# Kernel optimization log

Hardware: AMD Instinct MI355X
Metric: run time of the kernel (lower is better)

Reference implementation:

```python
import jax, jax.numpy as jnp
import numpy as np

D = 768      # d_model == d_patch (16*16*3)
DFF = 3072
NH = 12
DH = D // NH  # 64
P = 16
IMG = 224
HP = IMG // P  # 14
NP = HP * HP   # 196
L = NP + 1     # 197 with CLS
NL = 12        # layers (weights SHARED across layers, per original code)
NC = 1000


def _pos_enc(length, d):
    # Faithful to PositionalEncoding: even dims sin with exponent i, odd dims cos with exponent i-1
    pos = jnp.arange(length, dtype=jnp.float32)[:, None]          # [L,1]
    dim = jnp.arange(d)
    i = jnp.where(dim % 2 == 0, dim, (dim // 2) * 2).astype(jnp.float32)
    ang = pos / jnp.power(10000.0, i / d)                          # [L,D]
    return jnp.where(dim % 2 == 0, jnp.sin(ang), jnp.cos(ang))


def _ln(x, g, b, eps=1e-5):
    m = x.mean(-1, keepdims=True)
    v = x.var(-1, keepdims=True)
    return (x - m) / jnp.sqrt(v + eps) * g + b


def setup_inputs() -> dict:
    key = jax.random.key(0)
    ks = jax.random.split(key, 12)
    s = 0.02
    n = lambda k, shp: jax.random.normal(k, shp, jnp.float32) * s
    return {
        "x": jax.random.normal(ks[0], (32, 3, IMG, IMG), jnp.float32),
        "w_proj": n(ks[1], (D, D)), "b_proj": jnp.zeros((D,), jnp.float32),
        "cls_emb": jnp.zeros((1, 1, D), jnp.float32),
        "ln1_g": jnp.ones((D,), jnp.float32), "ln1_b": jnp.zeros((D,), jnp.float32),
        "w_qkv": n(ks[2], (3 * D, D)), "b_qkv": jnp.zeros((3 * D,), jnp.float32),
        "w_o": n(ks[3], (D, D)), "b_o": jnp.zeros((D,), jnp.float32),
        "ln2_g": jnp.ones((D,), jnp.float32), "ln2_b": jnp.zeros((D,), jnp.float32),
        "w_fc1": n(ks[4], (DFF, D)), "b_fc1": jnp.zeros((DFF,), jnp.float32),
        "w_fc2": n(ks[5], (D, DFF)), "b_fc2": jnp.zeros((D,), jnp.float32),
        "lnf_g": jnp.ones((D,), jnp.float32), "lnf_b": jnp.zeros((D,), jnp.float32),
        "w_h": n(ks[6], (D, D)), "b_h": jnp.zeros((D,), jnp.float32),
        "w_c": n(ks[7], (NC, D)), "b_c": jnp.zeros((NC,), jnp.float32),
    }


def reference(x, w_proj, b_proj, cls_emb, ln1_g, ln1_b, w_qkv, b_qkv, w_o, b_o,
              ln2_g, ln2_b, w_fc1, b_fc1, w_fc2, b_fc2, lnf_g, lnf_b,
              w_h, b_h, w_c, b_c):
    b = x.shape[0]
    # convert_to_patch: unfold -> channel-major patch features [b, NP, 3*P*P]
    patches = x.reshape(b, 3, HP, P, HP, P).transpose(0, 2, 4, 1, 3, 5).reshape(b, NP, 3 * P * P)
    emb = patches @ w_proj.T + b_proj                              # [b,NP,D]
    cls = jnp.broadcast_to(cls_emb, (b, 1, D))
    h = jnp.concatenate([cls, emb], axis=1) + _pos_enc(L, D)[None]  # [b,L,D]

    inv_sqrt_dk = 1.0 / jnp.sqrt(jnp.float32(DH))
    for _ in range(NL):  # SAME weights every layer (faithful to nn.Sequential of one object)
        y = _ln(h, ln1_g, ln1_b)
        qkv = y @ w_qkv.T + b_qkv                                   # [b,L,3D]
        # faithful non-standard head split: view(b,l,3*DH,NH).transpose -> [b,NH,L,3*DH]
        qkv = qkv.reshape(b, L, 3 * DH, NH).transpose(0, 3, 1, 2)
        q, k, v = jnp.split(qkv, 3, axis=-1)                        # each [b,NH,L,DH]
        attn = jax.nn.softmax(jnp.einsum('bhld,bhmd->bhlm', q, k) * inv_sqrt_dk, axis=-1)
        o = jnp.einsum('bhlm,bhmd->bhld', attn, v)                  # [b,NH,L,DH]
        o = o.transpose(0, 2, 1, 3).reshape(b, L, D)
        h = h + (o @ w_o.T + b_o)
        y = _ln(h, ln2_g, ln2_b)
        f = jax.nn.gelu(y @ w_fc1.T + b_fc1, approximate=False) @ w_fc2.T + b_fc2
        h = h + f

    rep = _ln(h[:, 0], lnf_g, lnf_b)                                # [b,D]
    hid = jnp.tanh(rep @ w_h.T + b_h)                               # is_pretrain=True
    return hid @ w_c.T + b_c                                        # [b,NC]
```

## Files before the change

### kernel.cpp

```cpp
#include <hip/hip_runtime.h>
#include <hip/hip_bf16.h>


typedef __bf16 bf16;
typedef __bf16 bf16x8 __attribute__((ext_vector_type(8)));
typedef __bf16 bf16x4 __attribute__((ext_vector_type(4)));
typedef float  f32x4  __attribute__((ext_vector_type(4)));

typedef __attribute__((address_space(1))) const unsigned int gu32;
typedef __attribute__((address_space(3))) unsigned int lu32;

static __device__ __forceinline__ f32x4 mfma_bf16(bf16x8 a, bf16x8 b, f32x4 c) {
  return __builtin_amdgcn_mfma_f32_16x16x32_bf16(a, b, c, 0, 0, 0);
}
static __device__ __forceinline__ void gll16(const bf16* g, bf16* l) {
  __builtin_amdgcn_global_load_lds((gu32*)g, (lu32*)l, 16, 0, 0);
}


__global__ __launch_bounds__(256) void f2b_k(const float* __restrict__ a, bf16* __restrict__ o, int n) {
  int i = blockIdx.x * 256 + threadIdx.x;
  if (i < n) o[i] = (bf16)a[i];
}

__global__ __launch_bounds__(256) void posenc_k(float* __restrict__ pos) {
  int l = blockIdx.x;
  for (int d = threadIdx.x; d < 768; d += 256) {
    int ieff = d & ~1;
    float ang = (float)l * expf(-(float)ieff * (9.210340371976184f / 768.0f));
    pos[l * 768 + d] = (d & 1) ? cosf(ang) : sinf(ang);
  }
}

__global__ __launch_bounds__(256) void patchify_k(const float* __restrict__ x, bf16* __restrict__ p) {
  int idx = blockIdx.x * 256 + threadIdx.x;
  int t = idx / 768, col = idx - t * 768;
  int b = t / 196, pp = t - b * 196;
  int ph = pp / 14, pw = pp - ph * 14;
  int c = col >> 8, r = col & 255, i = r >> 4, j = r & 15;
  p[idx] = (bf16)x[((b * 3 + c) * 224 + ph * 16 + i) * 224 + pw * 16 + j];
}

__global__ __launch_bounds__(256) void cls_k(float* __restrict__ h, const float* __restrict__ pos,
                                             const float* __restrict__ cls) {
  int b = blockIdx.x;
  for (int d = threadIdx.x; d < 768; d += 256)
    h[((size_t)b * 197) * 768 + d] = cls[d] + pos[d];
}

template<int PAD>
__global__ __launch_bounds__(256) void ln4_k(const float* __restrict__ x, const float* __restrict__ g,
                                             const float* __restrict__ bb, bf16* __restrict__ y,
                                             int nrows, int instride) {
  const int wave = threadIdx.x >> 6, lane = threadIdx.x & 63;
  const int row = blockIdx.x * 4 + wave;
  if (row >= nrows) return;
  const float4* x4 = (const float4*)(x + (size_t)row * instride);
  float4 v0 = x4[lane], v1 = x4[lane + 64], v2 = x4[lane + 128];
  float s  = v0.x + v0.y + v0.z + v0.w + v1.x + v1.y + v1.z + v1.w + v2.x + v2.y + v2.z + v2.w;
  float s2 = v0.x*v0.x + v0.y*v0.y + v0.z*v0.z + v0.w*v0.w
           + v1.x*v1.x + v1.y*v1.y + v1.z*v1.z + v1.w*v1.w
           + v2.x*v2.x + v2.y*v2.y + v2.z*v2.z + v2.w*v2.w;
  #pragma unroll
  for (int o = 1; o < 64; o <<= 1) { s += __shfl_xor(s, o); s2 += __shfl_xor(s2, o); }
  float m = s * (1.0f / 768.0f);
  float inv = rsqrtf(s2 * (1.0f / 768.0f) - m * m + 1e-5f);
  int orow = row;
  if (PAD) { int bq = row / 197; orow = row + bq * 3; }
  bf16* yr = y + (size_t)orow * 768;
  const float4* g4 = (const float4*)g;
  const float4* b4 = (const float4*)bb;
  #pragma unroll
  for (int i = 0; i < 3; ++i) {
    int idx = lane + i * 64;
    float4 vv = (i == 0) ? v0 : (i == 1) ? v1 : v2;
    float4 gv = g4[idx], bv = b4[idx];
    bf16x4 o;
    o[0] = (bf16)((vv.x - m) * inv * gv.x + bv.x);
    o[1] = (bf16)((vv.y - m) * inv * gv.y + bv.y);
    o[2] = (bf16)((vv.z - m) * inv * gv.z + bv.z);
    o[3] = (bf16)((vv.w - m) * inv * gv.w + bv.w);
    *(bf16x4*)(yr + idx * 4) = o;
  }
}

template<int BN, int EPI>
__global__ __launch_bounds__(256) void gemm2(
    const bf16* __restrict__ A, const bf16* __restrict__ B,
    int M, int N, int K, int ldc, const float* __restrict__ bias,
    const float* __restrict__ posw,
    float* __restrict__ outF, bf16* __restrict__ outB)
{
  constexpr int WN = (BN == 128) ? 64 : 32;
  constexpr int NI = WN / 16;
  constexpr int NB = BN / 32;
  __shared__ alignas(16) bf16 As[128 * 64];
  __shared__ alignas(16) bf16 Bs[BN * 64];
  const int tid = threadIdx.x;
  const int lane = tid & 63, wave = tid >> 6;
  const int wr = wave >> 1, wc = wave & 1;
  const int lrow = lane & 15, lgrp = lane >> 4;
  const int row0 = blockIdx.x * 128, col0 = blockIdx.y * BN;

  f32x4 acc[4][NI] = {};
  const bf16* Agb = A + (size_t)row0 * K;
  const bf16* Bgb = B + (size_t)col0 * K;
  const int srow = lane >> 3, schunk = lane & 7;
  const int nk = K >> 6;

  for (int kt = 0; kt < nk; ++kt) {
    const bf16* Ag = Agb + kt * 64;
    const bf16* Bg = Bgb + kt * 64;
    #pragma unroll
    for (int i = 0; i < 4; ++i) {
      int rr = (wave * 4 + i) * 8 + srow;
      int g = schunk ^ (rr & 7);
      gll16(Ag + (size_t)rr * K + g * 8, As + (wave * 4 + i) * 512);
    }
    #pragma unroll
    for (int i = 0; i < NB; ++i) {
      int rr = (wave * NB + i) * 8 + srow;
      int g = schunk ^ (rr & 7);
      gll16(Bg + (size_t)rr * K + g * 8, Bs + (wave * NB + i) * 512);
    }
    __syncthreads();
    #pragma unroll
    for (int kk = 0; kk < 2; ++kk) {
      bf16x8 af[4], bfr[NI];
      #pragma unroll
      for (int mi = 0; mi < 4; ++mi) {
        int r = wr * 64 + mi * 16 + lrow;
        af[mi] = *(const bf16x8*)(As + r * 64 + (((kk * 4 + lgrp) ^ (r & 7)) << 3));
      }
      #pragma unroll
      for (int ni = 0; ni < NI; ++ni) {
        int r = wc * WN + ni * 16 + lrow;
        bfr[ni] = *(const bf16x8*)(Bs + r * 64 + (((kk * 4 + lgrp) ^ (r & 7)) << 3));
      }
      #pragma unroll
      for (int mi = 0; mi < 4; ++mi)
        #pragma unroll
        for (int ni = 0; ni < NI; ++ni)
          acc[mi][ni] = mfma_bf16(af[mi], bfr[ni], acc[mi][ni]);
    }
    __syncthreads();
  }

  #pragma unroll
  for (int ni = 0; ni < NI; ++ni) {
    const int col = col0 + wc * WN + ni * 16 + lrow;
    float bs = 0.0f;
    if (EPI != 1) {
      if (EPI == 5) bs = (col < N) ? bias[col] : 0.0f;
      else          bs = bias[col];
    }
    #pragma unroll
    for (int mi = 0; mi < 4; ++mi) {
      const int rbase = row0 + wr * 64 + mi * 16 + (lgrp << 2);
      #pragma unroll
      for (int j = 0; j < 4; ++j) {
        const int t = rbase + j;
        if (EPI == 1) {
          float val = acc[mi][ni][j] + bias[t];
          if (t < 768) val *= 0.125f;
          outB[(size_t)t * ldc + col] = (bf16)val;
        } else {
          if (t >= M) continue;
          float val = acc[mi][ni][j] + bs;
          if (EPI == 0) {
            int b = t / 196, p = t - b * 196;
            outF[((size_t)(b * 197 + 1 + p)) * 768 + col] = val + posw[(size_t)(1 + p) * 768 + col];
          } else if (EPI == 2) {
            outF[(size_t)t * 768 + col] += val;
          } else if (EPI == 3) {
            outB[(size_t)t * 3072 + col] = (bf16)(0.5f * val * (1.0f + erff(val * 0.70710678118654752f)));
          } else if (EPI == 4) {
            outB[(size_t)t * 768 + col] = (bf16)tanhf(val);
          } else {
            if (col < N) outF[(size_t)t * ldc + col] = val;
          }
        }
      }
    }
  }
}

__global__ __launch_bounds__(256) void attn_k(const bf16* __restrict__ Ct, bf16* __restrict__ O) {
  __shared__ alignas(16) bf16 smem[40960];
  bf16* Ks = smem;
  bf16* QP = smem + 13312;
  bf16* Vs = smem + 27136;
  const int bh = blockIdx.x;
  const int b = bh / 12, hh = bh - b * 12;
  const int tid = threadIdx.x, lane = tid & 63, wave = tid >> 6;
  const int lrow = lane & 15, lgrp = lane >> 4;
  const size_t tc0 = (size_t)b * 200;

  for (int task = tid; task < 1600; task += 256) {
    int d = task / 25, lc = task - d * 25;
    int l0 = lc * 8;
    const size_t cb = tc0 + l0;
    bf16x8 qv = *(const bf16x8*)(Ct + ((size_t)(d * 12 + hh)) * 6400 + cb);
    bf16x8 kv = *(const bf16x8*)(Ct + ((size_t)(768 + d * 12 + hh)) * 6400 + cb);
    bf16x8 vv = *(const bf16x8*)(Ct + ((size_t)(1536 + d * 12 + hh)) * 6400 + cb);
    #pragma unroll
    for (int e = 0; e < 8; ++e) {
      int l = l0 + e;
      int sw = ((((d >> 3) ^ (l & 7)) << 3) | (d & 7));
      Ks[l * 64 + sw] = kv[e];
      QP[l * 64 + sw] = qv[e];
    }
    *(bf16x8*)(Vs + d * 216 + l0) = vv;
  }
  for (int t2 = tid; t2 < 64 * 16; t2 += 256) {
    int d = t2 >> 4, c = 200 + (t2 & 15);
    Vs[d * 216 + c] = (bf16)0.0f;
  }
  __syncthreads();

  bf16x8 qa0[4], qa1[4];
  #pragma unroll
  for (int ii = 0; ii < 4; ++ii) {
    int rt = wave + ii * 4;
    if (rt < 13) {
      int r = rt * 16 + lrow;
      qa0[ii] = *(const bf16x8*)(QP + r * 64 + ((lgrp ^ (r & 7)) << 3));
      qa1[ii] = *(const bf16x8*)(QP + r * 64 + (((4 + lgrp) ^ (r & 7)) << 3));
    }
  }
  __syncthreads();

  bf16* Pw = QP + wave * (16 * 216);
  const bf16x8 zv = {};

  #pragma unroll
  for (int ii = 0; ii < 4; ++ii) {
    const int rt = wave + ii * 4;
    if (rt >= 13) break;
    f32x4 sacc[13];
    #pragma unroll
    for (int ct = 0; ct < 13; ++ct) {
      const int kr = ct * 16 + lrow;
      bf16x8 b0 = *(const bf16x8*)(Ks + kr * 64 + ((lgrp ^ (kr & 7)) << 3));
      bf16x8 b1 = *(const bf16x8*)(Ks + kr * 64 + (((4 + lgrp) ^ (kr & 7)) << 3));
      f32x4 s = {};
      s = mfma_bf16(qa0[ii], b0, s);
      s = mfma_bf16(qa1[ii], b1, s);
      sacc[ct] = s;
    }
    float inv4[4];
    #pragma unroll
    for (int j = 0; j < 4; ++j) {
      const int prow = (lgrp << 2) + j;
      float mx = -3.0e38f;
      #pragma unroll
      for (int ct = 0; ct < 13; ++ct) {
        int c = ct * 16 + lrow;
        if (c < 197) mx = fmaxf(mx, sacc[ct][j]);
      }
      #pragma unroll
      for (int o = 1; o < 16; o <<= 1) mx = fmaxf(mx, __shfl_xor(mx, o));
      float sum = 0.0f;
      #pragma unroll
      for (int ct = 0; ct < 13; ++ct) {
        int c = ct * 16 + lrow;
        float p = (c < 197) ? __expf(sacc[ct][j] - mx) : 0.0f;
        sum += p;
        Pw[prow * 216 + c] = (bf16)p;
      }
      #pragma unroll
      for (int o = 1; o < 16; o <<= 1) sum += __shfl_xor(sum, o);
      inv4[j] = 1.0f / sum;
    }
    f32x4 oacc[4] = {};
    #pragma unroll
    for (int mc = 0; mc < 7; ++mc) {
      bf16x8 pa;
      if (mc < 6) {
        pa = *(const bf16x8*)(Pw + lrow * 216 + mc * 32 + (lgrp << 3));
      } else {
        pa = *(const bf16x8*)(Pw + lrow * 216 + 192 + ((lgrp & 1) << 3));
        if (lgrp >= 2) pa = zv;
      }
      #pragma unroll
      for (int n2 = 0; n2 < 4; ++n2) {
        const int vr = n2 * 16 + lrow;
        bf16x8 vb;
        if (mc < 6) vb = *(const bf16x8*)(Vs + vr * 216 + mc * 32 + (lgrp << 3));
        else        vb = *(const bf16x8*)(Vs + vr * 216 + 192 + ((lgrp & 1) << 3));
        oacc[n2] = mfma_bf16(pa, vb, oacc[n2]);
      }
    }
    #pragma unroll
    for (int n2 = 0; n2 < 4; ++n2) {
      const int d = n2 * 16 + lrow;
      #pragma unroll
      for (int j = 0; j < 4; ++j) {
        const int qrow = rt * 16 + (lgrp << 2) + j;
        if (qrow < 197)
          O[((size_t)b * 197 + qrow) * 768 + hh * 64 + d] = (bf16)(oacc[n2][j] * inv4[j]);
      }
    }
  }
}


extern "C" void kernel_launch(void* const* d_in, const int* in_sizes, int n_in,
                              void* d_out, int out_size, void* d_ws, size_t ws_size,
                              hipStream_t stream) {
  const float* x      = (const float*)d_in[0];
  const float* w_proj = (const float*)d_in[1];
  const float* b_proj = (const float*)d_in[2];
  const float* cls    = (const float*)d_in[3];
  const float* ln1g   = (const float*)d_in[4];
  const float* ln1b   = (const float*)d_in[5];
  const float* w_qkv  = (const float*)d_in[6];
  const float* b_qkv  = (const float*)d_in[7];
  const float* w_o    = (const float*)d_in[8];
  const float* b_o    = (const float*)d_in[9];
  const float* ln2g   = (const float*)d_in[10];
  const float* ln2b   = (const float*)d_in[11];
  const float* w_fc1  = (const float*)d_in[12];
  const float* b_fc1  = (const float*)d_in[13];
  const float* w_fc2  = (const float*)d_in[14];
  const float* b_fc2  = (const float*)d_in[15];
  const float* lnfg   = (const float*)d_in[16];
  const float* lnfb   = (const float*)d_in[17];
  const float* w_h    = (const float*)d_in[18];
  const float* b_h    = (const float*)d_in[19];
  const float* w_c    = (const float*)d_in[20];
  const float* b_c    = (const float*)d_in[21];
  float* out = (float*)d_out;

  uint8_t* ws = (uint8_t*)d_ws;
  size_t off = 0;
  auto alloc = [&](size_t bytes) -> void* {
    void* p = ws + off; off += (bytes + 255) & ~(size_t)255; return p;
  };
  float* h    = (float*)alloc(6400ull * 768 * 4);
  bf16*  ybf  = (bf16*) alloc(6400ull * 768 * 2);
  bf16*  ct   = (bf16*) alloc(2304ull * 6400 * 2);
  bf16*  ob   = (bf16*) alloc(6400ull * 768 * 2);
  bf16*  f1   = (bf16*) alloc(6400ull * 3072 * 2);
  float* pos  = (float*)alloc(197ull * 768 * 4);
  bf16* wprojB = (bf16*)alloc(768ull * 768 * 2);
  bf16* wqkvB  = (bf16*)alloc(2304ull * 768 * 2);
  bf16* woB    = (bf16*)alloc(768ull * 768 * 2);
  bf16* wfc1B  = (bf16*)alloc(3072ull * 768 * 2);
  bf16* wfc2B  = (bf16*)alloc(768ull * 3072 * 2);
  bf16* whB    = (bf16*)alloc(768ull * 768 * 2);
  bf16* wcB    = (bf16*)alloc(1024ull * 768 * 2);
  bf16* repB   = (bf16*)alloc(128ull * 768 * 2);
  bf16* hidB   = (bf16*)alloc(128ull * 768 * 2);
  bf16* patches = f1;

  f2b_k<<<(768 * 768 + 255) / 256, 256, 0, stream>>>(w_proj, wprojB, 768 * 768);
  f2b_k<<<(2304 * 768 + 255) / 256, 256, 0, stream>>>(w_qkv, wqkvB, 2304 * 768);
  f2b_k<<<(768 * 768 + 255) / 256, 256, 0, stream>>>(w_o, woB, 768 * 768);
  f2b_k<<<(3072 * 768 + 255) / 256, 256, 0, stream>>>(w_fc1, wfc1B, 3072 * 768);
  f2b_k<<<(768 * 3072 + 255) / 256, 256, 0, stream>>>(w_fc2, wfc2B, 768 * 3072);
  f2b_k<<<(768 * 768 + 255) / 256, 256, 0, stream>>>(w_h, whB, 768 * 768);
  f2b_k<<<(1000 * 768 + 255) / 256, 256, 0, stream>>>(w_c, wcB, 1000 * 768);
  posenc_k<<<197, 256, 0, stream>>>(pos);
  patchify_k<<<6272 * 768 / 256, 256, 0, stream>>>(x, patches);
  gemm2<64, 0><<<dim3(49, 12), 256, 0, stream>>>(patches, wprojB, 6272, 768, 768, 768,
                                                 b_proj, pos, h, nullptr);
  cls_k<<<32, 256, 0, stream>>>(h, pos, cls);

  for (int layer = 0; layer < 12; ++layer) {
    ln4_k<1><<<1576, 256, 0, stream>>>(h, ln1g, ln1b, ybf, 6304, 768);
    gemm2<128, 1><<<dim3(18, 50), 256, 0, stream>>>(wqkvB, ybf, 2304, 6400, 768, 6400,
                                                    b_qkv, nullptr, nullptr, ct);
    attn_k<<<384, 256, 0, stream>>>(ct, ob);
    gemm2<64, 2><<<dim3(50, 12), 256, 0, stream>>>(ob, woB, 6304, 768, 768, 768,
                                                   b_o, nullptr, h, nullptr);
    ln4_k<0><<<1576, 256, 0, stream>>>(h, ln2g, ln2b, ybf, 6304, 768);
    gemm2<128, 3><<<dim3(50, 24), 256, 0, stream>>>(ybf, wfc1B, 6304, 3072, 768, 3072,
                                                    b_fc1, nullptr, nullptr, f1);
    gemm2<64, 2><<<dim3(50, 12), 256, 0, stream>>>(f1, wfc2B, 6304, 768, 3072, 768,
                                                   b_fc2, nullptr, h, nullptr);
  }

  ln4_k<0><<<8, 256, 0, stream>>>(h, lnfg, lnfb, repB, 32, 197 * 768);
  gemm2<64, 4><<<dim3(1, 12), 256, 0, stream>>>(repB, whB, 32, 768, 768, 768,
                                                b_h, nullptr, nullptr, hidB);
  gemm2<64, 5><<<dim3(1, 16), 256, 0, stream>>>(hidB, wcB, 32, 1000, 768, 1000,
                                                b_c, nullptr, out, nullptr);
}
```

Baseline: 2.761 ms.

## Add 256x256-tile 8-wave GEMM with double-buffered LDS for QKV and FC1

Adds a new GEMM kernel that uses 512 threads and 256x256 output tiles, double-buffers A and B in LDS through direct global-to-LDS loads, and splits the staging into quarters interleaved with MFMA work. Wave priority is raised around the MFMA bursts. The QKV projection and FC1 (with GELU) are routed to it, and those epilogues are removed from the old kernel. The aim is more data reuse per tile and better overlap of loads with compute. The cost is 128 KB of LDS and heavy register use. The grids are also coarser, with 225 and 300 blocks, which may leave some CUs idle. FC1 reads rows past M=6304 up to 6400 from the padded buffers.

```diff
diff --git a/kernel.cpp b/kernel.cpp
--- a/kernel.cpp
+++ b/kernel.cpp
@@ -149,36 +149,133 @@
   #pragma unroll
   for (int ni = 0; ni < NI; ++ni) {
     const int col = col0 + wc * WN + ni * 16 + lrow;
-    float bs = 0.0f;
-    if (EPI != 1) {
-      if (EPI == 5) bs = (col < N) ? bias[col] : 0.0f;
-      else          bs = bias[col];
-    }
+    float bs = (EPI == 5) ? ((col < N) ? bias[col] : 0.0f) : bias[col];
     #pragma unroll
     for (int mi = 0; mi < 4; ++mi) {
       const int rbase = row0 + wr * 64 + mi * 16 + (lgrp << 2);
+      #pragma unroll
+      for (int j = 0; j < 4; ++j) {
+        const int t = rbase + j;
+        if (t >= M) continue;
+        float val = acc[mi][ni][j] + bs;
+        if (EPI == 0) {
+          int b = t / 196, p = t - b * 196;
+          outF[((size_t)(b * 197 + 1 + p)) * 768 + col] = val + posw[(size_t)(1 + p) * 768 + col];
+        } else if (EPI == 2) {
+          outF[(size_t)t * 768 + col] += val;
+        } else if (EPI == 4) {
+          outB[(size_t)t * 768 + col] = (bf16)tanhf(val);
+        } else {
+          if (col < N) outF[(size_t)t * ldc + col] = val;
+        }
+      }
+    }
+  }
+}
+
+template<int EPI>
+__global__ __launch_bounds__(512, 2) void gemm8(
+    const bf16* __restrict__ A, const bf16* __restrict__ B,
+    int M, int N, int K, int ldc, const float* __restrict__ bias,
+    bf16* __restrict__ outB)
+{
+  __shared__ alignas(16) bf16 smem[2 * 2 * 256 * 64];
+  const int tid = threadIdx.x;
+  const int lane = tid & 63, wave = tid >> 6;
+  const int wm = wave >> 2, wn = wave & 3;
+  const int lrow = lane & 15, lgrp = lane >> 4;
+  const int row0 = blockIdx.x * 256, col0 = blockIdx.y * 256;
+
+  f32x4 acc[8][4] = {};
+  const int srow = lane >> 3, schunk = lane & 7;
+  const int nk = K >> 6;
+  const bf16* Agb = A + (size_t)row0 * K;
+  const bf16* Bgb = B + (size_t)col0 * K;
+
+  auto stage_half = [&](int s, int mat, int h, int kt) {
+    const bf16* G = (mat == 0 ? Agb : Bgb) + kt * 64;
+    bf16* Lb = smem + (s * 2 + mat) * (256 * 64) + h * (128 * 64);
+    #pragma unroll
+    for (int shot = 0; shot < 2; ++shot) {
+      int rloc = wave * 16 + shot * 8;
+      int rr = h * 128 + rloc + srow;
+      int g = schunk ^ (rr & 7);
+      gll16(G + (size_t)rr * K + g * 8, Lb + rloc * 64);
+    }
+  };
+
+  #pragma unroll
+  for (int h = 0; h < 4; ++h) stage_half(0, h >> 1, h & 1, 0);
+  asm volatile("s_waitcnt vmcnt(0)" ::: "memory");
+  __builtin_amdgcn_s_barrier();
+
+  bf16x8 bfrag[8];
+  for (int g = 0; g < nk; ++g) {
+    const int s = g & 1;
+    const bf16* Asl = smem + (s * 2 + 0) * (256 * 64);
+    const bf16* Bsl = smem + (s * 2 + 1) * (256 * 64);
+    #pragma unroll
+    for (int q = 0; q < 4; ++q) {
+      if (g + 1 < nk) {
+        stage_half(s ^ 1, q >> 1, q & 1, g + 1);
+        asm volatile("s_waitcnt vmcnt(2)" ::: "memory");
+      } else if (q == 0) {
+        asm volatile("s_waitcnt vmcnt(0)" ::: "memory");
+      }
+      __builtin_amdgcn_sched_barrier(0);
+      __builtin_amdgcn_s_barrier();
+      if (q == 0) {
+        #pragma unroll
+        for (int n = 0; n < 4; ++n)
+          #pragma unroll
+          for (int kk = 0; kk < 2; ++kk) {
+            int r = wn * 64 + n * 16 + lrow;
+            bfrag[n * 2 + kk] = *(const bf16x8*)(Bsl + r * 64 + (((kk * 4 + lgrp) ^ (r & 7)) << 3));
+          }
+      }
+      bf16x8 af0k0, af0k1, af1k0, af1k1;
+      {
+        int r0 = wm * 128 + (q * 2) * 16 + lrow;
+        int r1 = wm * 128 + (q * 2 + 1) * 16 + lrow;
+        af0k0 = *(const bf16x8*)(Asl + r0 * 64 + (((0 + lgrp) ^ (r0 & 7)) << 3));
+        af0k1 = *(const bf16x8*)(Asl + r0 * 64 + (((4 + lgrp) ^ (r0 & 7)) << 3));
+        af1k0 = *(const bf16x8*)(Asl + r1 * 64 + (((0 + lgrp) ^ (r1 & 7)) << 3));
+        af1k1 = *(const bf16x8*)(Asl + r1 * 64 + (((4 + lgrp) ^ (r1 & 7)) << 3));
+      }
+      __builtin_amdgcn_s_setprio(1);
+      #pragma unroll
+      for (int n = 0; n < 4; ++n) {
+        acc[q * 2 + 0][n] = mfma_bf16(af0k0, bfrag[n * 2 + 0], acc[q * 2 + 0][n]);
+        acc[q * 2 + 1][n] = mfma_bf16(af1k0, bfrag[n * 2 + 0], acc[q * 2 + 1][n]);
+      }
+      #pragma unroll
+      for (int n = 0; n < 4; ++n) {
+        acc[q * 2 + 0][n] = mfma_bf16(af0k1, bfrag[n * 2 + 1], acc[q * 2 + 0][n]);
+        acc[q * 2 + 1][n] = mfma_bf16(af1k1, bfrag[n * 2 + 1], acc[q * 2 + 1][n]);
+      }
+      __builtin_amdgcn_s_setprio(0);
+      __builtin_amdgcn_s_barrier();
+    }
+  }
+
+  #pragma unroll
+  for (int nf = 0; nf < 4; ++nf) {
+    const int col = col0 + wn * 64 + nf * 16 + lrow;
+    float bs = (EPI == 3) ? bias[col] : 0.0f;
+    #pragma unroll
+    for (int mf = 0; mf < 8; ++mf) {
+      const int rbase = row0 + wm * 128 + mf * 16 + (lgrp << 2);
       #pragma unroll
       for (int j = 0; j < 4; ++j) {
         const int t = rbase + j;
         if (EPI == 1) {
-          float val = acc[mi][ni][j] + bias[t];
+          float val = acc[mf][nf][j] + bias[t];
           if (t < 768) val *= 0.125f;
           outB[(size_t)t * ldc + col] = (bf16)val;
         } else {
           if (t >= M) continue;
-          float val = acc[mi][ni][j] + bs;
-          if (EPI == 0) {
-            int b = t / 196, p = t - b * 196;
-            outF[((size_t)(b * 197 + 1 + p)) * 768 + col] = val + posw[(size_t)(1 + p) * 768 + col];
-          } else if (EPI == 2) {
-            outF[(size_t)t * 768 + col] += val;
-          } else if (EPI == 3) {
-            outB[(size_t)t * 3072 + col] = (bf16)(0.5f * val * (1.0f + erff(val * 0.70710678118654752f)));
-          } else if (EPI == 4) {
-            outB[(size_t)t * 768 + col] = (bf16)tanhf(val);
-          } else {
-            if (col < N) outF[(size_t)t * ldc + col] = val;
-          }
+          float val = acc[mf][nf][j] + bs;
+          outB[(size_t)t * 3072 + col] = (bf16)(0.5f * val * (1.0f + erff(val * 0.70710678118654752f)));
         }
       }
     }
@@ -369,14 +466,14 @@
 
   for (int layer = 0; layer < 12; ++layer) {
     ln4_k<1><<<1576, 256, 0, stream>>>(h, ln1g, ln1b, ybf, 6304, 768);
-    gemm2<128, 1><<<dim3(18, 50), 256, 0, stream>>>(wqkvB, ybf, 2304, 6400, 768, 6400,
-                                                    b_qkv, nullptr, nullptr, ct);
+    gemm8<1><<<dim3(9, 25), 512, 0, stream>>>(wqkvB, ybf, 2304, 6400, 768, 6400,
+                                              b_qkv, ct);
     attn_k<<<384, 256, 0, stream>>>(ct, ob);
     gemm2<64, 2><<<dim3(50, 12), 256, 0, stream>>>(ob, woB, 6304, 768, 768, 768,
                                                    b_o, nullptr, h, nullptr);
     ln4_k<0><<<1576, 256, 0, stream>>>(h, ln2g, ln2b, ybf, 6304, 768);
-    gemm2<128, 3><<<dim3(50, 24), 256, 0, stream>>>(ybf, wfc1B, 6304, 3072, 768, 3072,
-                                                    b_fc1, nullptr, nullptr, f1);
+    gemm8<3><<<dim3(25, 12), 512, 0, stream>>>(ybf, wfc1B, 6304, 3072, 768, 3072,
+                                               b_fc1, f1);
     gemm2<64, 2><<<dim3(50, 12), 256, 0, stream>>>(f1, wfc2B, 6304, 768, 3072, 768,
                                                    b_fc2, nullptr, h, nullptr);
   }
```

Result: slower. 3.226 ms (+16.8%).
